# Performance work log

Hardware: AMD Instinct MI355X
Metric: run time of the kernel (lower is better)

## Reference

```python
import jax, jax.numpy as jnp
import numpy as np

NUM_EMBEDDINGS = 1024
EMBEDDING_DIM = 64
COMMITMENT_COST = 0.25


def setup_inputs() -> dict:
    key = jax.random.key(0)
    k1, k2 = jax.random.split(key)
    z = jax.random.normal(k1, (32, EMBEDDING_DIM, 64, 64), dtype=jnp.float32)
    # nn.Embedding weight initialized uniform(-1/K, 1/K)
    lim = 1.0 / NUM_EMBEDDINGS
    codebook = jax.random.uniform(k2, (NUM_EMBEDDINGS, EMBEDDING_DIM),
                                  dtype=jnp.float32, minval=-lim, maxval=lim)
    return {"z": z, "codebook": codebook}


def reference(z, codebook):
    B, D, H, W = z.shape
    # (B, D, H, W) -> (B*H*W, D)
    z_flat = jnp.transpose(z, (0, 2, 3, 1)).reshape(-1, D)
    # squared L2 distances to all codebook entries: (N, K)
    distances = (jnp.sum(z_flat * z_flat, axis=1, keepdims=True)
                 + jnp.sum(codebook * codebook, axis=1)
                 - 2.0 * (z_flat @ codebook.T))
    encoding_indices = jnp.argmin(distances, axis=1)  # (N,)
    z_q = codebook[encoding_indices]                   # (N, D) gather
    z_q = jnp.transpose(z_q.reshape(B, H, W, D), (0, 3, 1, 2))
    vq_loss = jnp.mean((jax.lax.stop_gradient(z_q) - z) ** 2)
    commitment_loss = jnp.mean((z_q - jax.lax.stop_gradient(z)) ** 2)
    loss = vq_loss + COMMITMENT_COST * commitment_loss
    # straight-through estimator
    z_q_st = z + jax.lax.stop_gradient(z_q - z)
    return z_q_st, loss, encoding_indices.reshape(B, H * W)
```

## Files before the change

### kernel.cpp

```cpp
#include <hip/hip_runtime.h>

#define ZN 131072
#define DD 64
#define KK 1024
#define BSTRIDE 262144
#define DSTRIDE 4096
#define ZQ_ELEMS 8388608
#define TAU 2e-4f

#define WS_CSQ_OFF   32
#define WS_ROW_OFF   528416
#define WS_PACK_OFF  1052704
#define WS_CBB_OFF   2363408
#define WS_CAND_OFF  2625552

typedef __attribute__((ext_vector_type(8))) short short8;
typedef __attribute__((ext_vector_type(4))) float f32x4;

__device__ __forceinline__ unsigned short f2bf_rne(float x) {
    unsigned u = __float_as_uint(x);
    return (unsigned short)((u + 0x7fffu + ((u >> 16) & 1u)) >> 16);
}

__device__ __forceinline__ float np_sumsq64(const float* a) {
    float r0 = __fmul_rn(a[0], a[0]), r1 = __fmul_rn(a[1], a[1]);
    float r2 = __fmul_rn(a[2], a[2]), r3 = __fmul_rn(a[3], a[3]);
    float r4 = __fmul_rn(a[4], a[4]), r5 = __fmul_rn(a[5], a[5]);
    float r6 = __fmul_rn(a[6], a[6]), r7 = __fmul_rn(a[7], a[7]);
#pragma unroll
    for (int i = 8; i < 64; i += 8) {
        r0 = __fadd_rn(r0, __fmul_rn(a[i + 0], a[i + 0]));
        r1 = __fadd_rn(r1, __fmul_rn(a[i + 1], a[i + 1]));
        r2 = __fadd_rn(r2, __fmul_rn(a[i + 2], a[i + 2]));
        r3 = __fadd_rn(r3, __fmul_rn(a[i + 3], a[i + 3]));
        r4 = __fadd_rn(r4, __fmul_rn(a[i + 4], a[i + 4]));
        r5 = __fadd_rn(r5, __fmul_rn(a[i + 5], a[i + 5]));
        r6 = __fadd_rn(r6, __fmul_rn(a[i + 6], a[i + 6]));
        r7 = __fadd_rn(r7, __fmul_rn(a[i + 7], a[i + 7]));
    }
    return __fadd_rn(__fadd_rn(__fadd_rn(r0, r1), __fadd_rn(r2, r3)),
                     __fadd_rn(__fadd_rn(r4, r5), __fadd_rn(r6, r7)));
}

__global__ __launch_bounds__(256) void vq_prep(const float* __restrict__ cb,
                                               float* __restrict__ csq,
                                               unsigned short* __restrict__ cbB,
                                               double* __restrict__ acc,
                                               unsigned* __restrict__ ctrs) {
    if (blockIdx.x == 0 && threadIdx.x < 2) {
        if (threadIdx.x == 0) *acc = 0.0;
        ctrs[threadIdx.x] = 0u;
    }
    int k = blockIdx.x * 256 + threadIdx.x;
    const float* cp = cb + k * DD;
    csq[k] = np_sumsq64(cp);
    int ct = k >> 4, col = k & 15;
#pragma unroll
    for (int d = 0; d < DD; ++d) {
        float c = cp[d];
        unsigned short hi = f2bf_rne(c);
        float hf = __uint_as_float((unsigned)hi << 16);
        unsigned short lo = f2bf_rne(c - hf);
        int s = d >> 5, lg = (d >> 3) & 3, j = d & 7;
        int lane = col + 16 * lg;
        int base = ct * 2048 + s * 512 + lane * 8 + j;
        cbB[base] = hi;
        cbB[base + 1024] = lo;
    }
}

#define MFMA_DIST(P, Q, A_H0, A_H1, A_L0, A_L1, B0, B1, B2, B3)               \
    P = __builtin_amdgcn_mfma_f32_16x16x32_bf16(A_H0, B0, P, 0, 0, 0);        \
    Q = __builtin_amdgcn_mfma_f32_16x16x32_bf16(A_H0, B2, Q, 0, 0, 0);        \
    P = __builtin_amdgcn_mfma_f32_16x16x32_bf16(A_H1, B1, P, 0, 0, 0);        \
    Q = __builtin_amdgcn_mfma_f32_16x16x32_bf16(A_H1, B3, Q, 0, 0, 0);        \
    P = __builtin_amdgcn_mfma_f32_16x16x32_bf16(A_L0, B0, P, 0, 0, 0);        \
    Q = __builtin_amdgcn_mfma_f32_16x16x32_bf16(A_L1, B1, Q, 0, 0, 0);

__global__ __attribute__((amdgpu_waves_per_eu(2))) __launch_bounds__(256)
void vq_scan(const float* __restrict__ z,
             const unsigned short* __restrict__ cbB,
             const float* __restrict__ csq,
             float* __restrict__ idxf_out,
             unsigned* __restrict__ ctrs,
             unsigned* __restrict__ rowinfo,
             unsigned short* __restrict__ candbuf,
             unsigned candcap,
             unsigned long long* __restrict__ pack) {
    __shared__ __align__(16) unsigned short aFrag[4][2][2][64][8];
    __shared__ float scsq[1024];
    __shared__ int candCnt[64];
    __shared__ unsigned short candK[64][16];
    __shared__ unsigned char ovfF[64];

    int t = threadIdx.x;
    int n0 = blockIdx.x * 64;
    int b = n0 >> 12, p0 = n0 & 4095;

    for (int i = t; i < 1024; i += 256) scsq[i] = csq[i];
    if (t < 64) pack[n0 + t] = ~0ull;

    {
        int r = t & 63, gb = t >> 6;
        const float* zp = z + (size_t)b * BSTRIDE + p0 + r;
#pragma unroll
        for (int gg = 0; gg < 2; ++gg) {
            int g = (gb << 1) | gg;
            short8 hi8, lo8;
#pragma unroll
            for (int i2 = 0; i2 < 8; ++i2) {
                float v = zp[(size_t)(8 * g + i2) * DSTRIDE];
                unsigned short h = f2bf_rne(v);
                float hf = __uint_as_float((unsigned)h << 16);
                hi8[i2] = (short)h;
                lo8[i2] = (short)f2bf_rne(v - hf);
            }
            int rt = r >> 4, s = g >> 2, lane = (r & 15) + 16 * (g & 3);
            *(short8*)&aFrag[rt][s][0][lane][0] = hi8;
            *(short8*)&aFrag[rt][s][1][lane][0] = lo8;
        }
    }
    __syncthreads();

    int l = t & 63;
    int colcode = l & 15;
    int w = __builtin_amdgcn_readfirstlane(t >> 6);

    short8 aH0 = *(const short8*)&aFrag[w][0][0][l][0];
    short8 aH1 = *(const short8*)&aFrag[w][1][0][l][0];
    short8 aL0 = *(const short8*)&aFrag[w][0][1][l][0];
    short8 aL1 = *(const short8*)&aFrag[w][1][1][l][0];

    float m1[4], m2[4];
    int bst[4];
#pragma unroll
    for (int r = 0; r < 4; ++r) {
        m1[r] = 3.4e38f;
        m2[r] = 3.4e38f;
        bst[r] = 0;
    }

    const unsigned short* bpb = cbB + (l << 3);
    short8 nb0 = *(const short8*)(bpb);
    short8 nb1 = *(const short8*)(bpb + 512);
    short8 nb2 = *(const short8*)(bpb + 1024);
    short8 nb3 = *(const short8*)(bpb + 1536);
    for (int ph = 0; ph < 8; ++ph) {
        __syncthreads();
#pragma unroll 2
        for (int c8 = 0; c8 < 8; ++c8) {
            int ct = (ph << 3) | c8;
            short8 b0 = nb0, b1 = nb1, b2 = nb2, b3 = nb3;
            if (ct < 63) {
                const unsigned short* np = bpb + (ct + 1) * 2048;
                nb0 = *(const short8*)(np);
                nb1 = *(const short8*)(np + 512);
                nb2 = *(const short8*)(np + 1024);
                nb3 = *(const short8*)(np + 1536);
            }
            float cs = scsq[(ct << 4) + colcode];
            int code = (ct << 4) + colcode;
            f32x4 p = {0.f, 0.f, 0.f, 0.f}, q = {0.f, 0.f, 0.f, 0.f};
            MFMA_DIST(p, q, aH0, aH1, aL0, aL1, b0, b1, b2, b3)
#pragma unroll
            for (int r = 0; r < 4; ++r) {
                float dist = fmaf(-2.f, p[r] + q[r], cs);
                bool lt = dist < m1[r];
                m2[r] = lt ? m1[r] : fminf(m2[r], dist);
                bst[r] = lt ? code : bst[r];
                m1[r] = lt ? dist : m1[r];
            }
        }
    }

    int g = l >> 4;
#pragma unroll
    for (int r = 0; r < 4; ++r) {
        float v = m1[r];
        v = fminf(v, __shfl_xor(v, 1, 64));
        v = fminf(v, __shfl_xor(v, 2, 64));
        v = fminf(v, __shfl_xor(v, 4, 64));
        v = fminf(v, __shfl_xor(v, 8, 64));
        float thr = v + TAU;
        bool mine = (m1[r] < thr);
        unsigned long long bal1 = __ballot(mine);
        unsigned long long bal2 = __ballot(m2[r] < thr);
        unsigned slice1 = (unsigned)((bal1 >> (16 * g)) & 0xFFFFull);
        unsigned slice2 = (unsigned)((bal2 >> (16 * g)) & 0xFFFFull);
        int row = (w << 4) + (g << 2) + r;
        if (mine) {
            int pos = __popc(slice1 & ((1u << colcode) - 1u));
            candK[row][pos] = (unsigned short)bst[r];
        }
        if (colcode == 0) {
            candCnt[row] = __popc(slice1);
            ovfF[row] = (slice2 != 0u) ? 1 : 0;
        }
    }
    __syncthreads();

    if (t < 64) {
        int cnt = candCnt[t];
        bool ovf = (ovfF[t] != 0);
        bool resolved = (cnt == 1 && !ovf);
        if (resolved) idxf_out[n0 + t] = (float)candK[t][0];
        bool amb = !resolved;
        unsigned long long mb = __ballot(amb);
        int tot = __popcll(mb);
        unsigned base = 0;
        if (t == 0 && tot) base = atomicAdd(&ctrs[1], (unsigned)tot);
        base = __shfl(base, 0, 64);
        if (amb) {
            unsigned slot = base + (unsigned)__popcll(mb & ((1ull << t) - 1ull));
            bool fits = (slot < candcap);
            unsigned useOvf = (ovf || !fits) ? 1u : 0u;
            unsigned ccnt = useOvf ? 0u : (unsigned)cnt;
            rowinfo[slot] = (unsigned)(n0 + t) | (ccnt << 17) | (useOvf << 22);
            if (!useOvf)
                for (int i = 0; i < cnt; ++i)
                    candbuf[slot * 16 + i] = candK[t][i];
        }
    }
}

__device__ __forceinline__ unsigned long long ref_pack_c(const float* zr,
                                                         const float* cp,
                                                         float zsqn, float csqk,
                                                         unsigned k) {
    double a0 = 0.0, a1 = 0.0, a2 = 0.0, a3 = 0.0;
#pragma unroll
    for (int d = 0; d < DD; d += 4) {
        a0 = fma((double)zr[d + 0], (double)cp[d + 0], a0);
        a1 = fma((double)zr[d + 1], (double)cp[d + 1], a1);
        a2 = fma((double)zr[d + 2], (double)cp[d + 2], a2);
        a3 = fma((double)zr[d + 3], (double)cp[d + 3], a3);
    }
    double dot = (a0 + a1) + (a2 + a3);
    float twoC = (float)(2.0 * dot);
    float dist = __fsub_rn(__fadd_rn(zsqn, csqk), twoC);
    unsigned ub = __float_as_uint(dist);
    ub = (ub & 0x80000000u) ? ~ub : (ub | 0x80000000u);
    return ((unsigned long long)ub << 32) | k;
}

__global__ __launch_bounds__(256) void vq_refine2(
    const float* __restrict__ z,
    const float* __restrict__ cb,
    const float* __restrict__ csq,
    const unsigned* __restrict__ ctrs,
    const unsigned* __restrict__ rowinfo,
    const unsigned short* __restrict__ candbuf,
    unsigned long long* __restrict__ pack) {
    __shared__ float zrow[4][64];
    int l = threadIdx.x & 63;
    int wv = threadIdx.x >> 6;
    unsigned nrows = ctrs[1];
    unsigned nwaves = gridDim.x * 4;

    for (unsigned s = blockIdx.x * 4 + wv; s < nrows; s += nwaves) {
        unsigned info = rowinfo[s];
        unsigned n = info & 0x1FFFFu;
        unsigned cnt = (info >> 17) & 0x1Fu;
        bool ovf = ((info >> 22) & 1u) != 0u;
        int b = n >> 12, p = n & 4095;
        const float* zp = z + (size_t)b * BSTRIDE + p;

        zrow[wv][l] = zp[(size_t)l * DSTRIDE];
        asm volatile("s_waitcnt lgkmcnt(0)" ::: "memory");

        float zsqn = np_sumsq64(&zrow[wv][0]);

        unsigned long long pk = ~0ull;
        if (ovf) {
#pragma unroll
            for (int c = 0; c < 16; ++c) {
                unsigned k = (unsigned)(c * 64 + l);
                unsigned long long v =
                    ref_pack_c(&zrow[wv][0], cb + k * DD, zsqn, csq[k], k);
                pk = (v < pk) ? v : pk;
            }
        } else if ((unsigned)l < cnt) {
            unsigned k = candbuf[s * 16 + l];
            pk = ref_pack_c(&zrow[wv][0], cb + k * DD, zsqn, csq[k], k);
        }
#pragma unroll
        for (int off = 32; off; off >>= 1) {
            unsigned long long o =
                (unsigned long long)__shfl_xor((long long)pk, off, 64);
            pk = (o < pk) ? o : pk;
        }
        if (l == 0) pack[n] = pk;
    }
}

__global__ __launch_bounds__(256) void vq_gather_loss(const float* __restrict__ z,
                                                      const float* __restrict__ cb,
                                                      const unsigned long long* __restrict__ pack,
                                                      float* __restrict__ idxf,
                                                      float* __restrict__ zq_out,
                                                      float* __restrict__ loss_out,
                                                      double* __restrict__ acc,
                                                      unsigned* __restrict__ ctrs) {
    __shared__ float scb[256][65];
    __shared__ int skey[256];
    __shared__ float partial[4];

    int t = threadIdx.x;
    int n = blockIdx.x * 256 + t;

    unsigned long long pk = pack[n];
    int k = (pk != ~0ull) ? (int)(unsigned)(pk & 1023ull) : (int)idxf[n];
    idxf[n] = (float)k;
    skey[t] = k;
    __syncthreads();

    int l = t & 63, wv = t >> 6;
    for (int i = 0; i < 64; ++i) {
        int row = (wv << 6) + i;
        scb[row][l] = cb[skey[row] * DD + l];
    }
    __syncthreads();

    int b = n >> 12, p = n & 4095;
    const float* zp = z + (size_t)b * BSTRIDE + p;
    float* qp = zq_out + (size_t)b * BSTRIDE + p;

    float s = 0.f;
#pragma unroll
    for (int d = 0; d < DD; ++d) {
        float qv = scb[t][d];
        float diff = qv - zp[(size_t)d * DSTRIDE];
        s = fmaf(diff, diff, s);
        qp[(size_t)d * DSTRIDE] = qv;
    }

#pragma unroll
    for (int off = 32; off; off >>= 1) s += __shfl_down(s, off, 64);
    if (l == 0) partial[wv] = s;
    __syncthreads();
    if (t == 0) {
        float tt = (partial[0] + partial[1]) + (partial[2] + partial[3]);
        atomicAdd(acc, (double)tt);
        __threadfence();
        unsigned v = atomicAdd(&ctrs[0], 1u);
        if (v == gridDim.x - 1) {
            __threadfence();
            double s2 = atomicAdd(acc, 0.0);
            *loss_out = (float)(1.25 * s2 / (double)ZQ_ELEMS);
        }
    }
}

extern "C" void kernel_launch(void* const* d_in, const int* in_sizes, int n_in,
                              void* d_out, int out_size, void* d_ws, size_t ws_size,
                              hipStream_t stream) {
    const float* z = (const float*)d_in[0];
    const float* cb = (const float*)d_in[1];
    float* out = (float*)d_out;

    float* zq_out = out;
    float* loss_out = out + ZQ_ELEMS;
    float* idxf_out = out + ZQ_ELEMS + 1;

    char* ws = (char*)d_ws;
    double* acc = (double*)ws;
    unsigned* ctrs = (unsigned*)(ws + 8);
    float* csq = (float*)(ws + WS_CSQ_OFF);
    unsigned* rowinfo = (unsigned*)(ws + WS_ROW_OFF);
    unsigned long long* pack = (unsigned long long*)(ws + WS_PACK_OFF);
    unsigned short* cbB = (unsigned short*)(ws + WS_CBB_OFF);
    unsigned short* candbuf = (unsigned short*)(ws + WS_CAND_OFF);

    unsigned candcap = 0;
    if (ws_size > WS_CAND_OFF)
        candcap = (unsigned)((ws_size - WS_CAND_OFF) / 32);
    if (candcap > (unsigned)ZN) candcap = (unsigned)ZN;

    vq_prep<<<KK / 256, 256, 0, stream>>>(cb, csq, cbB, acc, ctrs);
    vq_scan<<<ZN / 64, 256, 0, stream>>>(z, cbB, csq, idxf_out, ctrs,
                                         rowinfo, candbuf, candcap, pack);
    vq_refine2<<<512, 256, 0, stream>>>(z, cb, csq, ctrs, rowinfo, candbuf, pack);
    vq_gather_loss<<<ZN / 256, 256, 0, stream>>>(z, cb, pack, idxf_out, zq_out,
                                                 loss_out, acc, ctrs);
}
```

Baseline: 311.5 us.

## Spread prep, refine and gather kernels across more threads and blocks

The codebook prep kernel now uses one thread per codebook element instead of one per row, so 64x more threads do the bf16 hi/lo split and scatter. The gather/loss kernel handles 64 rows per block, with four waves each covering a 16-dimension slice, which cuts shared memory use and quadruples the block count. The refine kernel grid grows from 512 to 2048 blocks. The aim is more parallelism and occupancy in these smaller kernels, at the cost of more blocks, extra loss atomics, and csq still being computed serially by the first 1024 prep threads.

Result: slower. 368.2 us (+18.2%).

```diff
diff --git a/kernel.cpp b/kernel.cpp
--- a/kernel.cpp
+++ b/kernel.cpp
@@ -47,26 +47,21 @@
                                                unsigned short* __restrict__ cbB,
                                                double* __restrict__ acc,
                                                unsigned* __restrict__ ctrs) {
-    if (blockIdx.x == 0 && threadIdx.x < 2) {
-        if (threadIdx.x == 0) *acc = 0.0;
-        ctrs[threadIdx.x] = 0u;
-    }
-    int k = blockIdx.x * 256 + threadIdx.x;
-    const float* cp = cb + k * DD;
-    csq[k] = np_sumsq64(cp);
+    int i = blockIdx.x * 256 + threadIdx.x;
+    if (i == 0) *acc = 0.0;
+    if (i < 2) ctrs[i] = 0u;
+    int k = i >> 6, d = i & 63;
+    float c = cb[i];
+    unsigned short hi = f2bf_rne(c);
+    float hf = __uint_as_float((unsigned)hi << 16);
+    unsigned short lo = f2bf_rne(c - hf);
     int ct = k >> 4, col = k & 15;
-#pragma unroll
-    for (int d = 0; d < DD; ++d) {
-        float c = cp[d];
-        unsigned short hi = f2bf_rne(c);
-        float hf = __uint_as_float((unsigned)hi << 16);
-        unsigned short lo = f2bf_rne(c - hf);
-        int s = d >> 5, lg = (d >> 3) & 3, j = d & 7;
-        int lane = col + 16 * lg;
-        int base = ct * 2048 + s * 512 + lane * 8 + j;
-        cbB[base] = hi;
-        cbB[base + 1024] = lo;
-    }
+    int s = d >> 5, lg = (d >> 3) & 3, j = d & 7;
+    int lane = col + 16 * lg;
+    int base = ct * 2048 + s * 512 + lane * 8 + j;
+    cbB[base] = hi;
+    cbB[base + 1024] = lo;
+    if (i < KK) csq[i] = np_sumsq64(cb + i * DD);
 }
 
 #define MFMA_DIST(P, Q, A_H0, A_H1, A_L0, A_L1, B0, B1, B2, B3)               \
@@ -301,34 +296,38 @@
                                                       float* __restrict__ loss_out,
                                                       double* __restrict__ acc,
                                                       unsigned* __restrict__ ctrs) {
-    __shared__ float scb[256][65];
-    __shared__ int skey[256];
+    __shared__ float scb[64][65];
+    __shared__ int skey[64];
     __shared__ float partial[4];
 
     int t = threadIdx.x;
-    int n = blockIdx.x * 256 + t;
-
-    unsigned long long pk = pack[n];
-    int k = (pk != ~0ull) ? (int)(unsigned)(pk & 1023ull) : (int)idxf[n];
-    idxf[n] = (float)k;
-    skey[t] = k;
-    __syncthreads();
-
-    int l = t & 63, wv = t >> 6;
-    for (int i = 0; i < 64; ++i) {
-        int row = (wv << 6) + i;
-        scb[row][l] = cb[skey[row] * DD + l];
-    }
-    __syncthreads();
-
-    int b = n >> 12, p = n & 4095;
-    const float* zp = z + (size_t)b * BSTRIDE + p;
-    float* qp = zq_out + (size_t)b * BSTRIDE + p;
+    int n0 = blockIdx.x * 64;
+    int b = n0 >> 12, p0 = n0 & 4095;
+
+    if (t < 64) {
+        int n = n0 + t;
+        unsigned long long pk = pack[n];
+        int k = (pk != ~0ull) ? (int)(unsigned)(pk & 1023ull) : (int)idxf[n];
+        idxf[n] = (float)k;
+        skey[t] = k;
+    }
+    __syncthreads();
+
+    for (int e = t; e < 4096; e += 256) {
+        int row = e >> 6, lane = e & 63;
+        scb[row][lane] = cb[skey[row] * DD + lane];
+    }
+    __syncthreads();
+
+    int r = t & 63, dg = t >> 6;
+    const float* zp = z + (size_t)b * BSTRIDE + p0 + r;
+    float* qp = zq_out + (size_t)b * BSTRIDE + p0 + r;
 
     float s = 0.f;
 #pragma unroll
-    for (int d = 0; d < DD; ++d) {
-        float qv = scb[t][d];
+    for (int i = 0; i < 16; ++i) {
+        int d = dg * 16 + i;
+        float qv = scb[r][d];
         float diff = qv - zp[(size_t)d * DSTRIDE];
         s = fmaf(diff, diff, s);
         qp[(size_t)d * DSTRIDE] = qv;
@@ -336,7 +335,7 @@
 
 #pragma unroll
     for (int off = 32; off; off >>= 1) s += __shfl_down(s, off, 64);
-    if (l == 0) partial[wv] = s;
+    if (r == 0) partial[dg] = s;
     __syncthreads();
     if (t == 0) {
         float tt = (partial[0] + partial[1]) + (partial[2] + partial[3]);
@@ -376,10 +375,10 @@
         candcap = (unsigned)((ws_size - WS_CAND_OFF) / 32);
     if (candcap > (unsigned)ZN) candcap = (unsigned)ZN;
 
-    vq_prep<<<KK / 256, 256, 0, stream>>>(cb, csq, cbB, acc, ctrs);
+    vq_prep<<<KK * DD / 256, 256, 0, stream>>>(cb, csq, cbB, acc, ctrs);
     vq_scan<<<ZN / 64, 256, 0, stream>>>(z, cbB, csq, idxf_out, ctrs,
                                          rowinfo, candbuf, candcap, pack);
-    vq_refine2<<<512, 256, 0, stream>>>(z, cb, csq, ctrs, rowinfo, candbuf, pack);
-    vq_gather_loss<<<ZN / 256, 256, 0, stream>>>(z, cb, pack, idxf_out, zq_out,
-                                                 loss_out, acc, ctrs);
-}
+    vq_refine2<<<2048, 256, 0, stream>>>(z, cb, csq, ctrs, rowinfo, candbuf, pack);
+    vq_gather_loss<<<ZN / 64, 256, 0, stream>>>(z, cb, pack, idxf_out, zq_out,
+                                                loss_out, acc, ctrs);
+}
```
